# Optimization experiments

Hardware: AMD Instinct MI355X
Metric: run time of the kernel (lower is better)

## Reference

```python
import jax, jax.numpy as jnp
import numpy as np

L_COORD, L_WIDTH, L_EF, L_EXISTS, L_NOOBJ = 5.0, 2.0, 2.0, 2.0, 1.0
B, Q, N, C = 64, 300, 64, 6
EPS = 1e-6


def setup_inputs() -> dict:
    key = jax.random.key(0)
    k1, k2, k3, k4, k5, k6 = jax.random.split(key, 6)
    exists = jax.random.uniform(k1, (B, Q, 1), minval=0.01, maxval=0.99, dtype=jnp.float32)
    coords = jax.random.uniform(k2, (B, Q, 4), dtype=jnp.float32)
    width = jax.random.uniform(k3, (B, Q, 1), dtype=jnp.float32)
    ef_logits = jax.random.normal(k4, (B, Q, C), dtype=jnp.float32)
    gt_geom = jax.random.uniform(k5, (B, N, 5), dtype=jnp.float32)  # 4 coords + width
    gt_cls = jax.random.randint(k6, (B, N, 1), 0, C).astype(jnp.float32)
    tracks = jnp.concatenate([gt_geom, gt_cls], axis=-1)  # (B,N,6)
    track_mask = jnp.ones((B, N), dtype=bool)
    return {"exists": exists, "coords": coords, "width": width,
            "ef_logits": ef_logits, "tracks": tracks, "track_mask": track_mask}


def _lsa(cost):
    """Rectangular linear sum assignment (shortest augmenting path, scipy algo).
    cost: (n, m) with n <= m. Returns col4row: col assigned to each row."""
    cost = np.asarray(cost, dtype=np.float64)
    n, m = cost.shape
    u = np.zeros(n); v = np.zeros(m)
    path = np.full(m, -1, np.int64)
    col4row = np.full(n, -1, np.int64)
    row4col = np.full(m, -1, np.int64)
    for cur_row in range(n):
        shortest = np.full(m, np.inf)
        SR = np.zeros(n, bool); SC = np.zeros(m, bool)
        min_val = 0.0; i = cur_row; sink = -1
        while sink == -1:
            SR[i] = True
            rem = ~SC
            d = min_val + cost[i, rem] - u[i] - v[rem]
            sh = shortest[rem]
            upd = d < sh
            sh[upd] = d[upd]
            shortest[rem] = sh
            pth = path[rem]
            pth[upd] = i
            path[rem] = pth
            ridx = np.flatnonzero(rem)
            j = ridx[np.argmin(shortest[ridx])]
            min_val = shortest[j]
            SC[j] = True
            if row4col[j] == -1:
                sink = j
            else:
                i = row4col[j]
        u[cur_row] += min_val
        rows = np.flatnonzero(SR); rows = rows[rows != cur_row]
        u[rows] += min_val - shortest[col4row[rows]]
        cols = np.flatnonzero(SC)
        v[cols] -= min_val - shortest[cols]
        j = sink
        while True:
            i = path[j]
            row4col[j] = i
            col4row[i], j = j, col4row[i]
            if i == cur_row:
                break
    return col4row


def _np_log_softmax(x):
    mx = x.max(-1, keepdims=True)
    return x - mx - np.log(np.exp(x - mx).sum(-1, keepdims=True))


def _match_batch(exists, coords, width, ef_logits, tracks, track_mask):
    """Host-side Hungarian matching (mirrors the @torch.no_grad() _match).
    Returns (pidx, valid): matched pred index per GT slot and validity mask."""
    pe = np.clip(np.asarray(exists)[..., 0], EPS, 1.0 - EPS)  # (B,Q)
    co = np.asarray(coords); wi = np.asarray(width)
    lo = _np_log_softmax(np.asarray(ef_logits))                # (B,Q,C)
    tr = np.asarray(tracks); mk = np.asarray(track_mask)
    Bn, Nmax = tr.shape[0], tr.shape[1]
    pidx = np.zeros((Bn, Nmax), np.int32)
    valid = np.zeros((Bn, Nmax), bool)
    for b in range(Bn):
        n = int(mk[b].sum())
        if n == 0:
            continue
        g = tr[b, :n]
        cost_coord = np.abs(co[b][:, None, :] - g[None, :, :4]).sum(-1)   # (Q,n) L1 cdist
        cost_width = np.abs(wi[b][:, None, :] - g[None, :, 4:5]).sum(-1)
        cost_ef = -lo[b][:, g[:, 5].astype(np.int64)]                     # (Q,n)
        cost_exists = -np.log(pe[b] + 1e-8)[:, None]                      # (Q,1)
        cost = (L_COORD * cost_coord + L_WIDTH * cost_width
                + L_EF * cost_ef + L_EXISTS * cost_exists)
        pidx[b, :n] = _lsa(cost.T)  # match each GT row to a pred column
        valid[b, :n] = True
    return pidx, valid


def _loss(exists, coords, width, ef_logits, tracks, pidx, valid):
    Bn, Qn = exists.shape[0], exists.shape[1]
    pe = jnp.clip(exists[..., 0], EPS, 1.0 - EPS)  # (B,Q)
    bidx = jnp.arange(Bn)[:, None]
    vf = valid.astype(coords.dtype)                # (B,N)
    mc = coords[bidx, pidx]                        # (B,N,4)
    mw = width[bidx, pidx]                         # (B,N,1)
    ml = ef_logits[bidx, pidx]                     # (B,N,C)
    mpe = pe[bidx, pidx]                           # (B,N)
    gcoord = tracks[..., :4]
    gwidth = tracks[..., 4:5]
    gcls = tracks[..., 5].astype(jnp.int32)
    total_coord = (jnp.abs(mc - gcoord).sum(-1) * vf).sum()
    total_width = (jnp.abs(mw - gwidth).sum(-1) * vf).sum()
    logp = jax.nn.log_softmax(ml, axis=-1)
    nll = -jnp.take_along_axis(logp, gcls[..., None], axis=-1)[..., 0]
    total_ef = (nll * vf).sum()
    total_exists = (-jnp.log(mpe) * vf).sum()
    matched = jnp.zeros((Bn, Qn), jnp.int32).at[bidx, pidx].add(valid.astype(jnp.int32)) > 0
    total_noobj = jnp.where(matched, 0.0, -jnp.log(1.0 - pe)).sum()
    n_matched = jnp.maximum(valid.sum(), 1).astype(coords.dtype)
    n_unmatched = jnp.maximum(Bn * Qn - valid.sum(), 1).astype(coords.dtype)
    coord_loss = L_COORD * total_coord / n_matched
    width_loss = L_WIDTH * total_width / n_matched
    ef_loss = L_EF * total_ef / n_matched
    exists_loss = L_EXISTS * total_exists / n_matched
    noobj_loss = L_NOOBJ * total_noobj / n_unmatched
    total = coord_loss + width_loss + ef_loss + exists_loss + noobj_loss
    return jnp.stack([total, coord_loss, width_loss, ef_loss, exists_loss, noobj_loss])


def reference(exists, coords, width, ef_logits, tracks, track_mask):
    pidx_np, valid_np = _match_batch(exists, coords, width, ef_logits, tracks, track_mask)
    pidx = jnp.asarray(pidx_np)
    valid = jnp.asarray(valid_np)
    return _loss(exists, coords, width, ef_logits, tracks, pidx, valid)
```

## Files before the change

kernel.cpp:

```cpp
#include <hip/hip_runtime.h>
#include <math.h>
#include <float.h>

#define BATCH 64
#define Q 300
#define N 64
#define CLS 6
#define SLOTS 5
#define NT 256
#define CSTRIDE 320

__device__ __forceinline__ int readlane_i(int x, int l) {
    return __builtin_amdgcn_readlane(x, l);
}
__device__ __forceinline__ float readlane_f(float x, int l) {
    return __int_as_float(__builtin_amdgcn_readlane(__float_as_int(x), l));
}
template <int CTRL>
__device__ __forceinline__ float fdpp(float x) {
    return __int_as_float(
        __builtin_amdgcn_update_dpp(0, __float_as_int(x), CTRL, 0xf, 0xf, true));
}
template <int CTRL>
__device__ __forceinline__ float fmin_dpp(float x) { return fminf(x, fdpp<CTRL>(x)); }
__device__ __forceinline__ float wave_min(float x) {
    x = fmin_dpp<0xB1>(x);
    x = fmin_dpp<0x4E>(x);
    x = fmin_dpp<0x141>(x);
    x = fmin_dpp<0x140>(x);
    float r0 = readlane_f(x, 0),  r1 = readlane_f(x, 16),
          r2 = readlane_f(x, 32), r3 = readlane_f(x, 48);
    return fminf(fminf(r0, r1), fminf(r2, r3));
}

__global__ __launch_bounds__(NT, 1) void hml_fused_kernel(
    const float* __restrict__ exists,
    const float* __restrict__ coords,
    const float* __restrict__ width,
    const float* __restrict__ ef,
    const float* __restrict__ tracks,
    float* __restrict__ part,
    unsigned int* __restrict__ counter,
    float* __restrict__ out)
{
    const int b = blockIdx.x;
    const int tid = threadIdx.x;
    const int lane = tid & 63;
    const int wid = tid >> 6;
    const bool s4ok = (lane < (Q - 4 * 64));
    const float INF = __builtin_inff();

    __shared__ float s_u[N];
    __shared__ int   s_want[N];
    __shared__ int s_colowner[SLOTS * 64];
    __shared__ int s_matched[SLOTS * 64];
    __shared__ float s_cost[N * CSTRIDE];

    float co0[SLOTS], co1[SLOTS], co2[SLOTS], co3[SLOTS];
    float wi_[SLOTS], pe_[SLOTS], ec2_[SLOTS];
    float base_[CLS][SLOTS];
    #pragma unroll
    for (int s = 0; s < SLOTS; ++s) {
        const int col = lane + 64 * s;
        const bool valid = (col < Q);
        const int idx = valid ? (b * Q + col) : (b * Q);
        float e = exists[idx];
        float pe = fminf(fmaxf(e, 1e-6f), 1.0f - 1e-6f);
        pe_[s] = pe;
        float e2 = -2.0f * logf(pe + 1e-8f);
        ec2_[s] = e2;
        wi_[s] = width[idx];
        const float4 c4 = reinterpret_cast<const float4*>(coords)[idx];
        co0[s] = c4.x; co1[s] = c4.y; co2[s] = c4.z; co3[s] = c4.w;
        const float* lp = ef + (size_t)idx * CLS;
        float x0 = lp[0], x1 = lp[1], x2 = lp[2], x3 = lp[3], x4 = lp[4], x5 = lp[5];
        float mx = fmaxf(fmaxf(fmaxf(x0, x1), fmaxf(x2, x3)), fmaxf(x4, x5));
        float sum = expf(x0 - mx) + expf(x1 - mx) + expf(x2 - mx)
                  + expf(x3 - mx) + expf(x4 - mx) + expf(x5 - mx);
        float off = mx + logf(sum);
        base_[0][s] = fmaf(-2.0f, x0 - off, e2);
        base_[1][s] = fmaf(-2.0f, x1 - off, e2);
        base_[2][s] = fmaf(-2.0f, x2 - off, e2);
        base_[3][s] = fmaf(-2.0f, x3 - off, e2);
        base_[4][s] = fmaf(-2.0f, x4 - off, e2);
        base_[5][s] = fmaf(-2.0f, x5 - off, e2);
    }

    float g0r, g1r, g2r, g3r, g4r; int clsr;
    {
        const float* gp = tracks + ((size_t)b * N + lane) * 6;
        g0r = gp[0]; g1r = gp[1]; g2r = gp[2]; g3r = gp[3]; g4r = gp[4];
        clsr = (int)gp[5];
    }

    for (int t = 0; t < N / 4; ++t) {
        const int i = (N / 4) * wid + t;
        float g0 = readlane_f(g0r, i), g1 = readlane_f(g1r, i),
              g2 = readlane_f(g2r, i), g3 = readlane_f(g3r, i),
              g4 = readlane_f(g4r, i);
        int cls = readlane_i(clsr, i);
        float msk[SLOTS];
        #pragma unroll
        for (int s = 0; s < SLOTS; ++s) {
            const bool slotvalid = (s < SLOTS - 1) || s4ok;
            float t01 = (cls == 1) ? base_[1][s] : base_[0][s];
            float t23 = (cls == 3) ? base_[3][s] : base_[2][s];
            float t45 = (cls == 5) ? base_[5][s] : base_[4][s];
            float t03 = (cls >= 2) ? t23 : t01;
            float bb  = (cls >= 4) ? t45 : t03;
            float cc = fabsf(co0[s] - g0) + fabsf(co1[s] - g1)
                     + fabsf(co2[s] - g2) + fabsf(co3[s] - g3);
            float cost = fmaf(5.0f, cc, fmaf(2.0f, fabsf(wi_[s] - g4), bb));
            msk[s] = slotvalid ? cost : INF;
        }
        #pragma unroll
        for (int s = 0; s < SLOTS; ++s)
            s_cost[i * CSTRIDE + lane + 64 * s] = msk[s];
        float lbest = fminf(fminf(fminf(msk[0], msk[1]), fminf(msk[2], msk[3])), msk[4]);
        unsigned jc = 0x7fffffffu;
        #pragma unroll
        for (int s = SLOTS - 1; s >= 0; --s)
            if (msk[s] == lbest) jc = (unsigned)(lane + 64 * s);
        float gmin = wave_min(lbest);
        unsigned long long ball = __ballot(lbest == gmin);
        int winner = __ffsll(ball) - 1;
        int bj = readlane_i((int)jc, winner);
        if (lane == 0) { s_u[i] = gmin; s_want[i] = bj; }
    }
    __syncthreads();
    if (wid != 0) return;

    float u_r = s_u[lane];
    int want_ = s_want[lane];

    #pragma unroll
    for (int s = 0; s < SLOTS; ++s) s_colowner[lane + 64 * s] = 0x7fffffff;
    __threadfence_block();
    atomicMin(&s_colowner[want_], lane);
    __threadfence_block();
    int col4row_r = (s_colowner[want_] == lane) ? want_ : -1;

    float v_[SLOTS];
    #pragma unroll
    for (int s = 0; s < SLOTS; ++s) v_[s] = 0.0f;

    float shortest_[SLOTS];
    int path_[SLOTS];
    bool SC_[SLOTS];

    unsigned long long freeball = __ballot(col4row_r == -1);
    while (freeball) {
        const int cur = __ffsll(freeball) - 1;
        freeball &= (freeball - 1);

        #pragma unroll
        for (int s = 0; s < SLOTS; ++s) {
            shortest_[s] = INF;
            SC_[s] = (s == SLOTS - 1) ? !s4ok : false;
        }
        bool SRr = false;
        float minv = 0.0f;
        int i = cur;
        int sink;

        for (;;) {
            SRr = SRr || (lane == i);
            float muv = minv - readlane_f(u_r, i);
            const float* crow = s_cost + i * CSTRIDE + lane;

            float msk[SLOTS];
            #pragma unroll
            for (int s = 0; s < SLOTS; ++s) {
                if (!SC_[s]) {
                    float d = muv + crow[64 * s] - v_[s];
                    if (d < shortest_[s]) { shortest_[s] = d; path_[s] = i; }
                    msk[s] = shortest_[s];
                } else {
                    msk[s] = INF;
                }
            }
            float lbest = fminf(fminf(fminf(msk[0], msk[1]), fminf(msk[2], msk[3])), msk[4]);
            unsigned jc = 0x7fffffffu;
            #pragma unroll
            for (int s = SLOTS - 1; s >= 0; --s)
                if (msk[s] == lbest) jc = (unsigned)(lane + 64 * s);
            float gmin = wave_min(lbest);
            unsigned long long ball = __ballot(lbest == gmin);
            int winner = __ffsll(ball) - 1;
            int bj = readlane_i((int)jc, winner);
            minv = gmin;

            const int bl = bj & 63, bs = bj >> 6;
            #pragma unroll
            for (int s = 0; s < SLOTS; ++s)
                if (bs == s && lane == bl) SC_[s] = true;
            unsigned long long ball2 = __ballot(col4row_r == bj);
            if (ball2 == 0ull) { sink = bj; break; }
            i = __ffsll(ball2) - 1;
        }

        const float minval = minv;
        {
            int c = col4row_r;
            int cl = c & 63, cs = c >> 6;
            float t0 = __shfl(shortest_[0], cl), t1 = __shfl(shortest_[1], cl),
                  t2 = __shfl(shortest_[2], cl), t3 = __shfl(shortest_[3], cl),
                  t4 = __shfl(shortest_[4], cl);
            float shc = t0;
            shc = (cs == 1) ? t1 : shc;
            shc = (cs == 2) ? t2 : shc;
            shc = (cs == 3) ? t3 : shc;
            shc = (cs == 4) ? t4 : shc;
            if (lane == cur) u_r += minval;
            else if (SRr)    u_r += minval - shc;
        }
        #pragma unroll
        for (int s = 0; s < SLOTS; ++s) {
            const bool slotvalid = (s < SLOTS - 1) || s4ok;
            if (slotvalid && SC_[s]) v_[s] -= minval - shortest_[s];
        }
        int j = sink;
        for (;;) {
            const int jl = j & 63, js = j >> 6;
            int ii_sel = path_[0];
            ii_sel = (js == 1) ? path_[1] : ii_sel;
            ii_sel = (js == 2) ? path_[2] : ii_sel;
            ii_sel = (js == 3) ? path_[3] : ii_sel;
            ii_sel = (js == 4) ? path_[4] : ii_sel;
            int ii = readlane_i(ii_sel, jl);
            int t = readlane_i(col4row_r, ii);
            if (lane == ii) col4row_r = j;
            j = t;
            if (ii == cur) break;
        }
    }

    #pragma unroll
    for (int s = 0; s < SLOTS; ++s) s_matched[lane + 64 * s] = 0;
    __threadfence_block();
    s_matched[col4row_r] = 1;
    __threadfence_block();

    float pc, pw, pef, pex;
    {
        const int p = col4row_r;
        const int pl = p & 63, ps = p >> 6;
        #define GATH(dst, a0, a1, a2, a3, a4)                                   \
        {   float t0 = __shfl(a0, pl), t1 = __shfl(a1, pl), t2 = __shfl(a2, pl),\
                  t3 = __shfl(a3, pl), t4 = __shfl(a4, pl);                     \
            dst = t0;                                                           \
            dst = (ps == 1) ? t1 : dst;                                         \
            dst = (ps == 2) ? t2 : dst;                                         \
            dst = (ps == 3) ? t3 : dst;                                         \
            dst = (ps == 4) ? t4 : dst; }
        float mc0, mc1, mc2, mc3, mw, mpe, me2;
        GATH(mc0, co0[0], co0[1], co0[2], co0[3], co0[4])
        GATH(mc1, co1[0], co1[1], co1[2], co1[3], co1[4])
        GATH(mc2, co2[0], co2[1], co2[2], co2[3], co2[4])
        GATH(mc3, co3[0], co3[1], co3[2], co3[3], co3[4])
        GATH(mw,  wi_[0], wi_[1], wi_[2], wi_[3], wi_[4])
        GATH(mpe, pe_[0], pe_[1], pe_[2], pe_[3], pe_[4])
        GATH(me2, ec2_[0], ec2_[1], ec2_[2], ec2_[3], ec2_[4])
        float b0, b1, b2, b3, b4, b5;
        GATH(b0, base_[0][0], base_[0][1], base_[0][2], base_[0][3], base_[0][4])
        GATH(b1, base_[1][0], base_[1][1], base_[1][2], base_[1][3], base_[1][4])
        GATH(b2, base_[2][0], base_[2][1], base_[2][2], base_[2][3], base_[2][4])
        GATH(b3, base_[3][0], base_[3][1], base_[3][2], base_[3][3], base_[3][4])
        GATH(b4, base_[4][0], base_[4][1], base_[4][2], base_[4][3], base_[4][4])
        GATH(b5, base_[5][0], base_[5][1], base_[5][2], base_[5][3], base_[5][4])
        #undef GATH
        float mb = b0;
        mb = (clsr == 1) ? b1 : mb;
        mb = (clsr == 2) ? b2 : mb;
        mb = (clsr == 3) ? b3 : mb;
        mb = (clsr == 4) ? b4 : mb;
        mb = (clsr == 5) ? b5 : mb;
        pc = fabsf(mc0 - g0r) + fabsf(mc1 - g1r) + fabsf(mc2 - g2r) + fabsf(mc3 - g3r);
        pw = fabsf(mw - g4r);
        pef = (mb - me2) * 0.5f;
        pex = -logf(mpe);
    }
    float pno = 0.0f;
    #pragma unroll
    for (int s = 0; s < SLOTS; ++s) {
        const bool slotvalid = (s < SLOTS - 1) || s4ok;
        if (slotvalid && !s_matched[lane + 64 * s]) pno -= logf(1.0f - pe_[s]);
    }

    float vals[5] = {pc, pw, pef, pex, pno};
    #pragma unroll
    for (int k = 0; k < 5; ++k) {
        float x = vals[k];
        #pragma unroll
        for (int off = 1; off < 64; off <<= 1) x += __shfl_xor(x, off);
        vals[k] = x;
    }
    if (lane == 0) {
        #pragma unroll
        for (int k = 0; k < 5; ++k) atomicExch(&part[b * 5 + k], vals[k]);
    }
    __threadfence();
    unsigned int done = 0;
    if (lane == 0) done = atomicAdd(counter, 1u);
    done = __shfl(done, 0);
    if (done == BATCH - 1) {
        __threadfence();
        float s0 = atomicAdd(&part[lane * 5 + 0], 0.0f);
        float s1 = atomicAdd(&part[lane * 5 + 1], 0.0f);
        float s2 = atomicAdd(&part[lane * 5 + 2], 0.0f);
        float s3 = atomicAdd(&part[lane * 5 + 3], 0.0f);
        float s4 = atomicAdd(&part[lane * 5 + 4], 0.0f);
        #pragma unroll
        for (int off = 1; off < 64; off <<= 1) {
            s0 += __shfl_xor(s0, off);
            s1 += __shfl_xor(s1, off);
            s2 += __shfl_xor(s2, off);
            s3 += __shfl_xor(s3, off);
            s4 += __shfl_xor(s4, off);
        }
        if (lane == 0) {
            const float n_matched = 4096.0f;
            const float n_unmatched = 15104.0f;
            float coord = 5.0f * s0 / n_matched;
            float wloss = 2.0f * s1 / n_matched;
            float efl   = 2.0f * s2 / n_matched;
            float exl   = 2.0f * s3 / n_matched;
            float nol   = 1.0f * s4 / n_unmatched;
            out[0] = coord + wloss + efl + exl + nol;
            out[1] = coord;
            out[2] = wloss;
            out[3] = efl;
            out[4] = exl;
            out[5] = nol;
        }
    }
}

extern "C" void kernel_launch(void* const* d_in, const int* in_sizes, int n_in,
                              void* d_out, int out_size, void* d_ws, size_t ws_size,
                              hipStream_t stream) {
    const float* exists = (const float*)d_in[0];
    const float* coords = (const float*)d_in[1];
    const float* width  = (const float*)d_in[2];
    const float* ef     = (const float*)d_in[3];
    const float* tracks = (const float*)d_in[4];

    float* part = (float*)d_ws;
    unsigned int* counter = (unsigned int*)((char*)d_ws + BATCH * 5 * sizeof(float));
    (void)hipMemsetAsync(counter, 0, sizeof(unsigned int), stream);

    hml_fused_kernel<<<BATCH, NT, 0, stream>>>(exists, coords, width, ef, tracks,
                                               part, counter, (float*)d_out);
}
```

Baseline: 115.4 us.

## Replace greedy init with auction bidding rounds and transpose cost matrix layout

Replaces the greedy row-min initialization with up to ten auction-style bidding rounds in which each free row bids for its best column using the first and second best reduced costs. Winners update column prices in LDS and rows that get outbid are freed. The cost matrix is stored transposed (column-major, stride 65) so each lane can scan its row across all columns without bank conflicts. The goal is fewer free rows left for the serial augmenting-path phase. The bidding rounds add their own serial cost, and the mixed dual updates have to remain consistent with the augmentation that follows.

```diff
diff --git a/kernel.cpp b/kernel.cpp
--- a/kernel.cpp
+++ b/kernel.cpp
@@ -8,7 +8,9 @@
 #define CLS 6
 #define SLOTS 5
 #define NT 256
-#define CSTRIDE 320
+#define CTS 65
+#define BID_CAP 10
+
 
 __device__ __forceinline__ int readlane_i(int x, int l) {
     return __builtin_amdgcn_readlane(x, l);
@@ -50,11 +52,10 @@
     const bool s4ok = (lane < (Q - 4 * 64));
     const float INF = __builtin_inff();
 
-    __shared__ float s_u[N];
-    __shared__ int   s_want[N];
     __shared__ int s_colowner[SLOTS * 64];
     __shared__ int s_matched[SLOTS * 64];
-    __shared__ float s_cost[N * CSTRIDE];
+    __shared__ __align__(16) float v_lds[SLOTS * 64];
+    __shared__ float s_cT[Q * CTS];
 
     float co0[SLOTS], co1[SLOTS], co2[SLOTS], co3[SLOTS];
     float wi_[SLOTS], pe_[SLOTS], ec2_[SLOTS];
@@ -99,7 +100,6 @@
               g2 = readlane_f(g2r, i), g3 = readlane_f(g3r, i),
               g4 = readlane_f(g4r, i);
         int cls = readlane_i(clsr, i);
-        float msk[SLOTS];
         #pragma unroll
         for (int s = 0; s < SLOTS; ++s) {
             const bool slotvalid = (s < SLOTS - 1) || s4ok;
@@ -111,38 +111,74 @@
             float cc = fabsf(co0[s] - g0) + fabsf(co1[s] - g1)
                      + fabsf(co2[s] - g2) + fabsf(co3[s] - g3);
             float cost = fmaf(5.0f, cc, fmaf(2.0f, fabsf(wi_[s] - g4), bb));
-            msk[s] = slotvalid ? cost : INF;
-        }
-        #pragma unroll
-        for (int s = 0; s < SLOTS; ++s)
-            s_cost[i * CSTRIDE + lane + 64 * s] = msk[s];
-        float lbest = fminf(fminf(fminf(msk[0], msk[1]), fminf(msk[2], msk[3])), msk[4]);
-        unsigned jc = 0x7fffffffu;
-        #pragma unroll
-        for (int s = SLOTS - 1; s >= 0; --s)
-            if (msk[s] == lbest) jc = (unsigned)(lane + 64 * s);
-        float gmin = wave_min(lbest);
-        unsigned long long ball = __ballot(lbest == gmin);
-        int winner = __ffsll(ball) - 1;
-        int bj = readlane_i((int)jc, winner);
-        if (lane == 0) { s_u[i] = gmin; s_want[i] = bj; }
+            if (slotvalid) s_cT[(lane + 64 * s) * CTS + i] = cost;
+        }
     }
     __syncthreads();
     if (wid != 0) return;
 
-    float u_r = s_u[lane];
-    int want_ = s_want[lane];
-
-    #pragma unroll
-    for (int s = 0; s < SLOTS; ++s) s_colowner[lane + 64 * s] = 0x7fffffff;
+    float u_r = 0.0f;
+    int col4row_r = -1;
+
+    #pragma unroll
+    for (int s = 0; s < SLOTS; ++s) v_lds[lane + 64 * s] = 0.0f;
     __threadfence_block();
-    atomicMin(&s_colowner[want_], lane);
-    __threadfence_block();
-    int col4row_r = (s_colowner[want_] == lane) ? want_ : -1;
+
+    for (int round = 0; round < BID_CAP; ++round) {
+        #pragma unroll
+        for (int s = 0; s < SLOTS; ++s) s_colowner[lane + 64 * s] = 0x7fffffff;
+        __threadfence_block();
+
+        float m1a = INF, m2a = INF, m1b = INF, m2b = INF;
+        unsigned ja = 0u, jb = 1u;
+        for (int k = 0; k < Q / 4; ++k) {
+            float4 vv = *reinterpret_cast<const float4*>(&v_lds[4 * k]);
+            float c0 = s_cT[(4 * k + 0) * CTS + lane];
+            float c1 = s_cT[(4 * k + 1) * CTS + lane];
+            float c2 = s_cT[(4 * k + 2) * CTS + lane];
+            float c3 = s_cT[(4 * k + 3) * CTS + lane];
+            float r0 = c0 - vv.x, r1 = c1 - vv.y, r2 = c2 - vv.z, r3 = c3 - vv.w;
+            bool lt;
+            lt = r0 < m1a; m2a = lt ? m1a : fminf(m2a, r0);
+            ja = lt ? (unsigned)(4 * k)     : ja; m1a = lt ? r0 : m1a;
+            lt = r1 < m1b; m2b = lt ? m1b : fminf(m2b, r1);
+            jb = lt ? (unsigned)(4 * k + 1) : jb; m1b = lt ? r1 : m1b;
+            lt = r2 < m1a; m2a = lt ? m1a : fminf(m2a, r2);
+            ja = lt ? (unsigned)(4 * k + 2) : ja; m1a = lt ? r2 : m1a;
+            lt = r3 < m1b; m2b = lt ? m1b : fminf(m2b, r3);
+            jb = lt ? (unsigned)(4 * k + 3) : jb; m1b = lt ? r3 : m1b;
+        }
+        float m1 = fminf(m1a, m1b);
+        unsigned j1 = (m1b < m1a) ? jb : ja;
+        float m2 = fminf(fmaxf(m1a, m1b), fminf(m2a, m2b));
+
+        const unsigned mykey = (__float_as_uint(m1) & 0xFFFFFFC0u) | (unsigned)lane;
+        const bool wasfree = (col4row_r < 0);
+        if (wasfree) {
+            u_r = fmaxf(u_r, m1);
+            atomicMin(&s_colowner[j1], (int)mykey);
+        }
+        __threadfence_block();
+        const bool winner    = wasfree && (s_colowner[j1] == (int)mykey);
+        const bool displaced = (!wasfree) && (s_colowner[col4row_r] != 0x7fffffff);
+        if (winner) {
+            u_r = m2;
+            v_lds[j1] -= (m2 - m1);
+            col4row_r = (int)j1;
+        }
+        if (displaced) col4row_r = -1;
+        __threadfence_block();
+        unsigned long long fb = __ballot(col4row_r == -1);
+        if (fb == 0ull || __popcll(fb) <= 2) break;
+    }
 
     float v_[SLOTS];
-    #pragma unroll
-    for (int s = 0; s < SLOTS; ++s) v_[s] = 0.0f;
+    int cb[SLOTS];
+    #pragma unroll
+    for (int s = 0; s < SLOTS; ++s) {
+        v_[s] = v_lds[lane + 64 * s];
+        cb[s] = (lane + 64 * s) * CTS;
+    }
 
     float shortest_[SLOTS];
     int path_[SLOTS];
@@ -166,13 +202,12 @@
         for (;;) {
             SRr = SRr || (lane == i);
             float muv = minv - readlane_f(u_r, i);
-            const float* crow = s_cost + i * CSTRIDE + lane;
 
             float msk[SLOTS];
             #pragma unroll
             for (int s = 0; s < SLOTS; ++s) {
                 if (!SC_[s]) {
-                    float d = muv + crow[64 * s] - v_[s];
+                    float d = muv + s_cT[cb[s] + i] - v_[s];
                     if (d < shortest_[s]) { shortest_[s] = d; path_[s] = i; }
                     msk[s] = shortest_[s];
                 } else {
```

Result: slower. 137.0 us (+18.7%).
